# Kernel optimization log

Measured on AMD Instinct MI355X. Metric: run time of the kernel, lower is better.

## Reference

```python
import jax, jax.numpy as jnp
import numpy as np

B, L, H = 2, 1024, 1024   # batch, seq_len, hidden_size
NH, D, K = 16, 64, 4      # num_heads, head_dim, conv kernel
HD = NH * D


def setup_inputs() -> dict:
    key = jax.random.key(0)
    ks = jax.random.split(key, 12)
    s = 0.02  # LeCun-ish init scale as in the torch module
    return {
        "hidden_states": jax.random.normal(ks[0], (B, L, H), jnp.float32),
        "Wq": jax.random.normal(ks[1], (HD, H), jnp.float32) * s,
        "bq": jnp.zeros((HD,), jnp.float32),
        "Wk": jax.random.normal(ks[2], (HD, H), jnp.float32) * s,
        "bk": jnp.zeros((HD,), jnp.float32),
        "Wv": jax.random.normal(ks[3], (HD, H), jnp.float32) * s,
        "bv": jnp.zeros((HD,), jnp.float32),
        "Wa": jax.random.normal(ks[4], (NH, H), jnp.float32) * s,
        "Wb": jax.random.normal(ks[5], (NH, H), jnp.float32) * s,
        "Wconv": jax.random.normal(ks[6], (HD, 1, K), jnp.float32) * s,
        "Wo": jax.random.normal(ks[7], (H, HD), jnp.float32) * s,
        "bo": jnp.zeros((H,), jnp.float32),
    }


def _gated_delta(q, k, v, alpha, beta):
    # q,k,v: [B,L,NH,D]; alpha,beta: [B,L,NH]
    # S_t = S_{t-1} @ (alpha_t * (I - beta_t k_t k_t^T)) + beta_t v_t k_t^T ; o_t = S_t q_t
    eye = jnp.eye(q.shape[-1], dtype=q.dtype)

    def step(S, xs):
        q_t, k_t, v_t, a_t, b_t = xs  # [B,NH,D], [B,NH]
        kk = jnp.einsum('bhd,bhe->bhde', k_t, k_t)
        decay = a_t[..., None, None] * (eye - b_t[..., None, None] * kk)
        S = jnp.einsum('bhde,bhef->bhdf', S, decay) \
            + b_t[..., None, None] * jnp.einsum('bhd,bhe->bhde', v_t, k_t)
        o_t = jnp.einsum('bhde,bhe->bhd', S, q_t)
        return S, o_t

    xs = (jnp.moveaxis(q, 1, 0), jnp.moveaxis(k, 1, 0), jnp.moveaxis(v, 1, 0),
          jnp.moveaxis(alpha, 1, 0), jnp.moveaxis(beta, 1, 0))
    S0 = jnp.zeros((q.shape[0], q.shape[2], q.shape[3], q.shape[3]), q.dtype)
    _, outs = jax.lax.scan(step, S0, xs)  # [L,B,NH,D]
    return jnp.transpose(outs, (1, 2, 0, 3))  # [B,NH,L,D] (matches torch stack+transposes)


def reference(hidden_states, Wq, bq, Wk, bk, Wv, bv, Wa, Wb, Wconv, Wo, bo):
    Bc, Lc, Hc = hidden_states.shape
    q = (hidden_states @ Wq.T + bq).reshape(Bc, Lc, NH, D)
    k = (hidden_states @ Wk.T + bk).reshape(Bc, Lc, NH, D)
    v = (hidden_states @ Wv.T + bv).reshape(Bc, Lc, NH, D)
    alpha = jax.nn.sigmoid(hidden_states @ Wa.T)   # [B,L,NH]
    beta = jax.nn.softplus(hidden_states @ Wb.T)   # [B,L,NH]

    out = _gated_delta(q, k, v, alpha, beta)       # [B,NH,L,D]
    out = out.reshape(Bc, Lc, NH * D)              # replicates torch's reshape of [B,NH,L,D]
    x = jnp.transpose(out, (0, 2, 1))              # [B,HD,L]
    conv = jax.lax.conv_general_dilated(
        x, Wconv, window_strides=(1,), padding=[(K - 1, 0)],
        feature_group_count=NH * D, dimension_numbers=('NCH', 'OIH', 'NCH'))
    x = x + conv                                   # residual depthwise causal conv
    x = jnp.transpose(x, (0, 2, 1))                # [B,L,HD]
    return x @ Wo.T + bo                           # [B,L,H]; dropout is identity at eval
```

## Files before the change

### kernel.cpp

```cpp
#include <hip/hip_runtime.h>
#include <math.h>

#define BB 2
#define LL 1024
#define HH 1024
#define NH 16
#define DD 64
#define HD (NH * DD)
#define MM (BB * LL)
#define RCT 32
#define KEXT 3072
#define NBK 1088

typedef _Float16 f16x8 __attribute__((ext_vector_type(8)));
typedef _Float16 f16x4 __attribute__((ext_vector_type(4)));
typedef float f32x4 __attribute__((ext_vector_type(4)));

__device__ __forceinline__ void load_lds16(const void* g, void* l) {
    __builtin_amdgcn_global_load_lds(
        (const __attribute__((address_space(1))) void*)g,
        (__attribute__((address_space(3))) void*)l, 16, 0, 0);
}

__global__ __launch_bounds__(256) void convert_front(
    const float* __restrict__ hs,
    const float* __restrict__ Wq, const float* __restrict__ Wk,
    const float* __restrict__ Wv, const float* __restrict__ Wa,
    const float* __restrict__ Wb, const float* __restrict__ Wo,
    _Float16* __restrict__ Ae3,
    _Float16* __restrict__ Bk, _Float16* __restrict__ Bqv,
    _Float16* __restrict__ Be2)
{
    const int blk = blockIdx.x;
    const int t = threadIdx.x;

    if (blk < 2048) {
        float4 x = *(const float4*)(hs + (size_t)blk * 1024 + t * 4);
        x.x *= 16.f; x.y *= 16.f; x.z *= 16.f; x.w *= 16.f;
        f16x4 h, l;
        h[0] = (_Float16)x.x; l[0] = (_Float16)(x.x - (float)h[0]);
        h[1] = (_Float16)x.y; l[1] = (_Float16)(x.y - (float)h[1]);
        h[2] = (_Float16)x.z; l[2] = (_Float16)(x.z - (float)h[2]);
        h[3] = (_Float16)x.w; l[3] = (_Float16)(x.w - (float)h[3]);
        _Float16* base = Ae3 + (size_t)blk * KEXT + t * 4;
        *(f16x4*)(base)        = h;
        *(f16x4*)(base + 1024) = l;
        *(f16x4*)(base + 2048) = h;
        return;
    }
    if (blk < 3136) {
        const int n = blk - 2048;
        const float* src = nullptr;
        if (n < 1024)      src = Wk + (size_t)n * 1024;
        else if (n < 1040) src = Wa + (size_t)(n - 1024) * 1024;
        else if (n < 1056) src = Wb + (size_t)(n - 1040) * 1024;
        float4 x = src ? *(const float4*)(src + t * 4)
                       : make_float4(0.f, 0.f, 0.f, 0.f);
        x.x *= 64.f; x.y *= 64.f; x.z *= 64.f; x.w *= 64.f;
        f16x4 h, l;
        h[0] = (_Float16)x.x; l[0] = (_Float16)(x.x - (float)h[0]);
        h[1] = (_Float16)x.y; l[1] = (_Float16)(x.y - (float)h[1]);
        h[2] = (_Float16)x.z; l[2] = (_Float16)(x.z - (float)h[2]);
        h[3] = (_Float16)x.w; l[3] = (_Float16)(x.w - (float)h[3]);
        _Float16* base = Bk + (size_t)n * KEXT + t * 4;
        *(f16x4*)(base)        = h;
        *(f16x4*)(base + 1024) = h;
        *(f16x4*)(base + 2048) = l;
        return;
    }
    if (blk < 5184) {
        const int n = blk - 3136;
        const float* src = (n < 1024) ? Wq + (size_t)n * 1024
                                      : Wv + (size_t)(n - 1024) * 1024;
        float4 x = *(const float4*)(src + t * 4);
        f16x4 h;
        h[0] = (_Float16)(x.x * 64.f);
        h[1] = (_Float16)(x.y * 64.f);
        h[2] = (_Float16)(x.z * 64.f);
        h[3] = (_Float16)(x.w * 64.f);
        *(f16x4*)(Bqv + (size_t)n * 1024 + t * 4) = h;
        return;
    }
    {
        const int n = blk - 5184;
        float4 x = *(const float4*)(Wo + (size_t)n * 1024 + t * 4);
        f16x4 h;
        h[0] = (_Float16)(x.x * 64.f);
        h[1] = (_Float16)(x.y * 64.f);
        h[2] = (_Float16)(x.z * 64.f);
        h[3] = (_Float16)(x.w * 64.f);
        *(f16x4*)(Be2 + (size_t)n * 1024 + t * 4) = h;
    }
}

__global__ __launch_bounds__(256) void mfma_gemm_proj(
    const _Float16* __restrict__ Ae3, const _Float16* __restrict__ Bk,
    const _Float16* __restrict__ Bqv,
    float* __restrict__ qkv, float* __restrict__ ab,
    const float* __restrict__ bq, const float* __restrict__ bk,
    const float* __restrict__ bv)
{
    __shared__ __align__(16) _Float16 As[2][128 * 32];
    __shared__ __align__(16) _Float16 Bs[2][128 * 32];

    const int blk = blockIdx.x;
    const int tid = threadIdx.x;
    const int wave = tid >> 6;
    const int lane = tid & 63;
    const int srow = lane >> 2;
    const int scol = (lane & 3) * 8;
    const int fm = lane & 15;
    const int fq = (lane >> 4) * 8;
    const int rquad = (lane >> 4) * 4;

    if (blk < 272) {
        const int bm = (blk / 17) * 128;
        const int bn = (blk % 17) * 64;
        const int wr = (wave >> 1) * 64;
        const int wc = (wave & 1) * 32;

        const _Float16* gA0 = Ae3 + (size_t)(bm + wave * 32 + srow) * KEXT + scol;
        const _Float16* gA1 = gA0 + (size_t)16 * KEXT;
        const _Float16* gB0 = Bk + (size_t)(bn + wave * 16 + srow) * KEXT + scol;
        _Float16* lA0_0 = &As[0][(wave * 32) * 32];
        _Float16* lA1_0 = &As[0][(wave * 32 + 16) * 32];
        _Float16* lB0_0 = &Bs[0][(wave * 16) * 32];
        _Float16* lA0_1 = &As[1][(wave * 32) * 32];
        _Float16* lA1_1 = &As[1][(wave * 32 + 16) * 32];
        _Float16* lB0_1 = &Bs[1][(wave * 16) * 32];

        f32x4 acc[4][2] = {};

        for (int k0 = 0; k0 < KEXT; k0 += 64) {
            load_lds16(gA0 + k0,      lA0_0);
            load_lds16(gA1 + k0,      lA1_0);
            load_lds16(gB0 + k0,      lB0_0);
            load_lds16(gA0 + k0 + 32, lA0_1);
            load_lds16(gA1 + k0 + 32, lA1_1);
            load_lds16(gB0 + k0 + 32, lB0_1);
            __syncthreads();

            #pragma unroll
            for (int s = 0; s < 2; ++s) {
                f16x8 a[4], b[2];
                #pragma unroll
                for (int mt = 0; mt < 4; ++mt)
                    a[mt] = *(const f16x8*)&As[s][(wr + mt * 16 + fm) * 32 + fq];
                #pragma unroll
                for (int nt = 0; nt < 2; ++nt)
                    b[nt] = *(const f16x8*)&Bs[s][(wc + nt * 16 + fm) * 32 + fq];
                #pragma unroll
                for (int mt = 0; mt < 4; ++mt)
                    #pragma unroll
                    for (int nt = 0; nt < 2; ++nt)
                        acc[mt][nt] = __builtin_amdgcn_mfma_f32_16x16x32_f16(
                            a[mt], b[nt], acc[mt][nt], 0, 0, 0);
            }
            __syncthreads();
        }

        #pragma unroll
        for (int mt = 0; mt < 4; ++mt) {
            #pragma unroll
            for (int nt = 0; nt < 2; ++nt) {
                const int col = bn + wc + nt * 16 + fm;
                #pragma unroll
                for (int i = 0; i < 4; ++i) {
                    const int row = bm + wr + mt * 16 + rquad + i;
                    float val = acc[mt][nt][i] * (1.0f / 1024.0f);
                    if (col < 1024)
                        qkv[(size_t)row * 3072 + 1024 + col] = val + bk[col];
                    else if (col < 1040)
                        ab[(size_t)row * 32 + (col - 1024)] =
                            1.f / (1.f + expf(-val));
                    else if (col < 1056)
                        ab[(size_t)row * 32 + 16 + (col - 1040)] =
                            fmaxf(val, 0.f) + log1pf(expf(-fabsf(val)));
                }
            }
        }
    } else {
        const int n = blk - 272;
        const int bm = (n / 16) * 128;
        const int bn = (n % 16) * 128;
        const int wr = (wave >> 1) * 64;
        const int wc = (wave & 1) * 64;

        const _Float16* gA0 = Ae3 + (size_t)(bm + wave * 32 + srow) * KEXT + scol;
        const _Float16* gA1 = gA0 + (size_t)16 * KEXT;
        const _Float16* gB0 = Bqv + (size_t)(bn + wave * 32 + srow) * 1024 + scol;
        const _Float16* gB1 = gB0 + (size_t)16 * 1024;
        _Float16* lA0_0 = &As[0][(wave * 32) * 32];
        _Float16* lA1_0 = &As[0][(wave * 32 + 16) * 32];
        _Float16* lB0_0 = &Bs[0][(wave * 32) * 32];
        _Float16* lB1_0 = &Bs[0][(wave * 32 + 16) * 32];
        _Float16* lA0_1 = &As[1][(wave * 32) * 32];
        _Float16* lA1_1 = &As[1][(wave * 32 + 16) * 32];
        _Float16* lB0_1 = &Bs[1][(wave * 32) * 32];
        _Float16* lB1_1 = &Bs[1][(wave * 32 + 16) * 32];

        f32x4 acc[4][4] = {};

        for (int k0 = 0; k0 < 1024; k0 += 64) {
            load_lds16(gA0 + k0,      lA0_0);
            load_lds16(gA1 + k0,      lA1_0);
            load_lds16(gB0 + k0,      lB0_0);
            load_lds16(gB1 + k0,      lB1_0);
            load_lds16(gA0 + k0 + 32, lA0_1);
            load_lds16(gA1 + k0 + 32, lA1_1);
            load_lds16(gB0 + k0 + 32, lB0_1);
            load_lds16(gB1 + k0 + 32, lB1_1);
            __syncthreads();

            #pragma unroll
            for (int s = 0; s < 2; ++s) {
                f16x8 a[4], b[4];
                #pragma unroll
                for (int mt = 0; mt < 4; ++mt)
                    a[mt] = *(const f16x8*)&As[s][(wr + mt * 16 + fm) * 32 + fq];
                #pragma unroll
                for (int nt = 0; nt < 4; ++nt)
                    b[nt] = *(const f16x8*)&Bs[s][(wc + nt * 16 + fm) * 32 + fq];
                #pragma unroll
                for (int mt = 0; mt < 4; ++mt)
                    #pragma unroll
                    for (int nt = 0; nt < 4; ++nt)
                        acc[mt][nt] = __builtin_amdgcn_mfma_f32_16x16x32_f16(
                            a[mt], b[nt], acc[mt][nt], 0, 0, 0);
            }
            __syncthreads();
        }

        #pragma unroll
        for (int mt = 0; mt < 4; ++mt) {
            #pragma unroll
            for (int nt = 0; nt < 4; ++nt) {
                const int col = bn + wc + nt * 16 + fm;
                #pragma unroll
                for (int i = 0; i < 4; ++i) {
                    const int row = bm + wr + mt * 16 + rquad + i;
                    float val = acc[mt][nt][i] * (1.0f / 1024.0f);
                    if (col < 1024)
                        qkv[(size_t)row * 3072 + col] = val + bq[col];
                    else
                        qkv[(size_t)row * 3072 + 1024 + col] = val + bv[col - 1024];
                }
            }
        }
    }
}

__global__ __launch_bounds__(256) void mfma_gemm_out(
    const _Float16* __restrict__ Ae2, const _Float16* __restrict__ Be2,
    float* __restrict__ outp, const float* __restrict__ bo)
{
    __shared__ __align__(16) _Float16 As[2][128 * 32];
    __shared__ __align__(16) _Float16 Bs[2][64 * 32];

    const int tid = threadIdx.x;
    const int wave = tid >> 6;
    const int lane = tid & 63;
    const int bm = blockIdx.y * 128;
    const int bn = blockIdx.x * 64;
    const int wr = (wave >> 1) * 64;
    const int wc = (wave & 1) * 32;

    const int srow = lane >> 2;
    const int scol = (lane & 3) * 8;
    const _Float16* gA0 = Ae2 + (size_t)(bm + wave * 32 + srow) * 1024 + scol;
    const _Float16* gA1 = gA0 + (size_t)16 * 1024;
    const _Float16* gB0 = Be2 + (size_t)(bn + wave * 16 + srow) * 1024 + scol;
    _Float16* lA0_0 = &As[0][(wave * 32) * 32];
    _Float16* lA1_0 = &As[0][(wave * 32 + 16) * 32];
    _Float16* lB0_0 = &Bs[0][(wave * 16) * 32];
    _Float16* lA0_1 = &As[1][(wave * 32) * 32];
    _Float16* lA1_1 = &As[1][(wave * 32 + 16) * 32];
    _Float16* lB0_1 = &Bs[1][(wave * 16) * 32];

    const int fm = lane & 15;
    const int fq = (lane >> 4) * 8;

    f32x4 acc[4][2] = {};

    for (int k0 = 0; k0 < 1024; k0 += 64) {
        load_lds16(gA0 + k0,      lA0_0);
        load_lds16(gA1 + k0,      lA1_0);
        load_lds16(gB0 + k0,      lB0_0);
        load_lds16(gA0 + k0 + 32, lA0_1);
        load_lds16(gA1 + k0 + 32, lA1_1);
        load_lds16(gB0 + k0 + 32, lB0_1);
        __syncthreads();

        #pragma unroll
        for (int s = 0; s < 2; ++s) {
            f16x8 a[4], b[2];
            #pragma unroll
            for (int mt = 0; mt < 4; ++mt)
                a[mt] = *(const f16x8*)&As[s][(wr + mt * 16 + fm) * 32 + fq];
            #pragma unroll
            for (int nt = 0; nt < 2; ++nt)
                b[nt] = *(const f16x8*)&Bs[s][(wc + nt * 16 + fm) * 32 + fq];
            #pragma unroll
            for (int mt = 0; mt < 4; ++mt)
                #pragma unroll
                for (int nt = 0; nt < 2; ++nt)
                    acc[mt][nt] = __builtin_amdgcn_mfma_f32_16x16x32_f16(
                        a[mt], b[nt], acc[mt][nt], 0, 0, 0);
        }
        __syncthreads();
    }

    const int rquad = (lane >> 4) * 4;
    #pragma unroll
    for (int mt = 0; mt < 4; ++mt) {
        #pragma unroll
        for (int nt = 0; nt < 2; ++nt) {
            const int col = bn + wc + nt * 16 + fm;
            #pragma unroll
            for (int i = 0; i < 4; ++i) {
                const int row = bm + wr + mt * 16 + rquad + i;
                outp[(size_t)row * 1024 + col] = acc[mt][nt][i] * 64.f + bo[col];
            }
        }
    }
}

template <int CTRL>
__device__ __forceinline__ float dpp_addf(float x) {
    int y = __builtin_amdgcn_update_dpp(0, __builtin_bit_cast(int, x),
                                        CTRL, 0xF, 0xF, true);
    return x + __builtin_bit_cast(float, y);
}
__device__ __forceinline__ float red16(float x) {
    x = dpp_addf<0xB1>(x);
    x = dpp_addf<0x4E>(x);
    x = dpp_addf<0x124>(x);
    x = dpp_addf<0x128>(x);
    return x;
}

__global__ __launch_bounds__(64) void gdn_recurrence(
    const float* __restrict__ qkv, const float* __restrict__ ab,
    float* __restrict__ att)
{
    __shared__ __align__(16) float ks[2][RCT][64];
    __shared__ __align__(16) float qs[2][RCT][64];
    __shared__ __align__(16) float vs_[2][RCT][4];
    __shared__ __align__(16) float gab[2][RCT][2];

    const int blk = blockIdx.x;
    const int bh = blk & 31;
    const int s  = blk >> 5;
    const int b  = bh >> 4;
    const int h  = bh & 15;
    const int lane = threadIdx.x;
    const int rl = lane >> 4;
    const int el = lane & 15;
    const int e0 = el * 4;
    const int r0 = s * 4;

    const float* qb  = qkv + (size_t)b * LL * 3072 + h * 64;
    const float* kb  = qb + 1024;
    const float* vb  = qb + 2048 + r0;
    const float* abp = ab + (size_t)b * LL * 32 + h;
    float* op = att + ((size_t)(b * NH + h) * DD + r0 + rl) * LL;

    const int st = lane >> 4;
    const int sd = (lane & 15) * 4;

    float S0 = 0.f, S1 = 0.f, S2 = 0.f, S3 = 0.f;

    {
        const size_t ro = (size_t)st * 3072 + sd;
        #pragma unroll
        for (int m = 0; m < 8; ++m) {
            load_lds16(kb + ro + (size_t)m * 4 * 3072, &ks[0][m * 4][0]);
            load_lds16(qb + ro + (size_t)m * 4 * 3072, &qs[0][m * 4][0]);
        }
        float4 pv = make_float4(0.f,0.f,0.f,0.f);
        if (lane < RCT) pv = *(const float4*)(vb + (size_t)lane * 3072);
        float pab = (lane < 32) ? abp[(size_t)lane * 32]
                                : abp[(size_t)(lane - 32) * 32 + 16];
        if (lane < RCT) *(float4*)&vs_[0][lane][0] = pv;
        if (lane < 32) gab[0][lane][0] = pab;
        else           gab[0][lane - 32][1] = pab;
    }
    __syncthreads();

    const int NCHUNK = LL / RCT;
    for (int c = 0; c < NCHUNK; ++c) {
        const int cur = c & 1, nxt = cur ^ 1;
        const bool more = (c + 1 < NCHUNK);

        float4 pv = make_float4(0.f,0.f,0.f,0.f);
        float pab = 0.f;
        if (more) {
            const size_t t0 = (size_t)(c + 1) * RCT;
            const size_t ro = (t0 + st) * 3072 + sd;
            #pragma unroll
            for (int m = 0; m < 8; ++m) {
                load_lds16(kb + ro + (size_t)m * 4 * 3072, &ks[nxt][m * 4][0]);
                load_lds16(qb + ro + (size_t)m * 4 * 3072, &qs[nxt][m * 4][0]);
            }
            if (lane < RCT) pv = *(const float4*)(vb + (t0 + lane) * 3072);
            pab = (lane < 32) ? abp[(t0 + lane) * 32]
                              : abp[(t0 + lane - 32) * 32 + 16];
        }

        float4 kr[4], qr[4];
        float vr[4];
        float2 abr[4];
        #pragma unroll
        for (int i = 0; i < 2; ++i) {
            kr[i] = *(const float4*)&ks[cur][i][e0];
            qr[i] = *(const float4*)&qs[cur][i][e0];
            vr[i] = vs_[cur][i][rl];
            abr[i] = *(const float2*)&gab[cur][i][0];
        }

        float o0 = 0.f, o1 = 0.f, o2 = 0.f;
        #pragma unroll 4
        for (int t = 0; t < RCT; ++t) {
            const int tf = (t + 2 < RCT) ? t + 2 : RCT - 1;
            kr[(t + 2) & 3] = *(const float4*)&ks[cur][tf][e0];
            qr[(t + 2) & 3] = *(const float4*)&qs[cur][tf][e0];
            vr[(t + 2) & 3] = vs_[cur][tf][rl];
            abr[(t + 2) & 3] = *(const float2*)&gab[cur][tf][0];

            const float4 kc = kr[t & 3];
            const float4 qc = qr[t & 3];
            const float vc = vr[t & 3];
            const float ac = abr[t & 3].x;
            const float bc = abr[t & 3].y;

            float p0 = fmaf(S1, kc.y, S0 * kc.x);
            float p1 = fmaf(S3, kc.w, S2 * kc.z);
            float sk = red16(p0 + p1);

            const float cf = bc * fmaf(-ac, sk, vc);

            S0 = fmaf(ac, S0, cf * kc.x);
            S1 = fmaf(ac, S1, cf * kc.y);
            S2 = fmaf(ac, S2, cf * kc.z);
            S3 = fmaf(ac, S3, cf * kc.w);

            float q0 = fmaf(S1, qc.y, S0 * qc.x);
            float q1 = fmaf(S3, qc.w, S2 * qc.z);
            float o = red16(q0 + q1);

            const int ph = t & 3;
            if (ph == 0) o0 = o;
            else if (ph == 1) o1 = o;
            else if (ph == 2) o2 = o;
            else if (el == 0)
                *(float4*)(op + c * RCT + t - 3) = make_float4(o0, o1, o2, o);
        }

        if (more) {
            if (lane < RCT) *(float4*)&vs_[nxt][lane][0] = pv;
            if (lane < 32) gab[nxt][lane][0] = pab;
            else           gab[nxt][lane - 32][1] = pab;
        }
        __syncthreads();
    }
}

__global__ __launch_bounds__(256) void conv_convert(
    const float* __restrict__ att, const float* __restrict__ Wconv,
    _Float16* __restrict__ Ae2)
{
    __shared__ float yt[112][68];
    const int lb = blockIdx.x;
    const int h  = blockIdx.y;
    const int b  = blockIdx.z;
    const int tid = threadIdx.x;

    {
        const int d = tid >> 2;
        const int part = tid & 3;
        const float* src  = att + ((size_t)(b * NH + h) * DD + d) * LL;
        const float* srcm = src - (size_t)DD * LL;
        #pragma unroll
        for (int m = 0; m < 7; ++m) {
            const int off = (part * 7 + m) * 4;
            const int lg = lb * 64 - 48 + off;
            float4 v;
            if (lg >= 0)      v = *(const float4*)(src + lg);
            else if (h > 0)   v = *(const float4*)(srcm + lg + 1024);
            else              v = make_float4(0.f, 0.f, 0.f, 0.f);
            yt[off + 0][d] = v.x; yt[off + 1][d] = v.y;
            yt[off + 2][d] = v.z; yt[off + 3][d] = v.w;
        }
    }
    __syncthreads();

    float4 w[4];
    #pragma unroll
    for (int k = 0; k < 4; ++k)
        w[k] = ((const float4*)Wconv)[tid * 4 + k];

    const int d0 = (tid & 15) * 4;
    const int lq = tid >> 4;
    const float sc = 1.f / 4096.f;

    #pragma unroll
    for (int rr = 0; rr < 4; ++rr) {
        const int ll = rr * 16 + lq;
        float y0[4], y1[4], y2[4], y3[4];
        *(float4*)y0 = *(const float4*)&yt[ll +  0][d0];
        *(float4*)y1 = *(const float4*)&yt[ll + 16][d0];
        *(float4*)y2 = *(const float4*)&yt[ll + 32][d0];
        *(float4*)y3 = *(const float4*)&yt[ll + 48][d0];
        f16x4 hi;
        #pragma unroll
        for (int k = 0; k < 4; ++k) {
            float acc = y3[k];
            acc = fmaf(w[k].x, y0[k], acc);
            acc = fmaf(w[k].y, y1[k], acc);
            acc = fmaf(w[k].z, y2[k], acc);
            acc = fmaf(w[k].w, y3[k], acc);
            hi[k] = (_Float16)(acc * sc);
        }
        const size_t row = (size_t)b * 1024 + h * 64 + lb * 4 + rr;
        *(f16x4*)(Ae2 + row * 1024 + tid * 4) = hi;
    }
}

extern "C" void kernel_launch(void* const* d_in, const int* in_sizes, int n_in,
                              void* d_out, int out_size, void* d_ws, size_t ws_size,
                              hipStream_t stream)
{
    const float* hs    = (const float*)d_in[0];
    const float* Wq    = (const float*)d_in[1];
    const float* bq    = (const float*)d_in[2];
    const float* Wk    = (const float*)d_in[3];
    const float* bk    = (const float*)d_in[4];
    const float* Wv    = (const float*)d_in[5];
    const float* bv    = (const float*)d_in[6];
    const float* Wa    = (const float*)d_in[7];
    const float* Wb    = (const float*)d_in[8];
    const float* Wconv = (const float*)d_in[9];
    const float* Wo    = (const float*)d_in[10];
    const float* bo    = (const float*)d_in[11];
    float* out = (float*)d_out;

    char* w = (char*)d_ws;
    float* qkv = (float*)w;        w += (size_t)MM * 3072 * 4;
    float* att = (float*)w;        w += (size_t)MM * 1024 * 4;
    float* ab  = (float*)w;        w += (size_t)MM * 32 * 4;
    _Float16* Ae3 = (_Float16*)w;  w += (size_t)MM * KEXT * 2;
    _Float16* Bk  = (_Float16*)w;  w += (size_t)NBK * KEXT * 2;
    _Float16* Bqv = (_Float16*)w;  w += (size_t)2048 * 1024 * 2;
    _Float16* Ae2 = (_Float16*)w;  w += (size_t)MM * 1024 * 2;
    _Float16* Be2 = (_Float16*)w;  w += (size_t)1024 * 1024 * 2;

    hipLaunchKernelGGL(convert_front, dim3(6208), dim3(256), 0, stream,
                       hs, Wq, Wk, Wv, Wa, Wb, Wo, Ae3, Bk, Bqv, Be2);

    hipLaunchKernelGGL(mfma_gemm_proj, dim3(528), dim3(256), 0, stream,
                       Ae3, Bk, Bqv, qkv, ab, bq, bk, bv);

    hipLaunchKernelGGL(gdn_recurrence, dim3(512), dim3(64), 0, stream, qkv, ab, att);

    hipLaunchKernelGGL(conv_convert, dim3(16, 16, BB), dim3(256), 0, stream,
                       att, Wconv, Ae2);

    hipLaunchKernelGGL(mfma_gemm_out, dim3(1024 / 64, MM / 128), dim3(256), 0, stream,
                       Ae2, Be2, out, bo);
}
```

Before: 292.8 us.

## Double-buffer LDS tiles to prefetch next K-step during MFMA compute

In the projection and output GEMM kernels, the LDS tiles become two ping-pong sets. The loads for the next 64-wide K step are issued before the MFMA work on the current step, so global-to-LDS traffic overlaps with compute instead of stalling at a barrier every iteration. The cost is twice the LDS per block (64 KB in the projection kernel), which may lower occupancy. The end-of-iteration barrier now also waits on the prefetch.

Measured after the change: 297.9 us. No clear change (+1.7%).

```diff
diff --git a/kernel.cpp b/kernel.cpp
--- a/kernel.cpp
+++ b/kernel.cpp
@@ -100,8 +100,8 @@
     const float* __restrict__ bq, const float* __restrict__ bk,
     const float* __restrict__ bv)
 {
-    __shared__ __align__(16) _Float16 As[2][128 * 32];
-    __shared__ __align__(16) _Float16 Bs[2][128 * 32];
+    __shared__ __align__(16) _Float16 As[2][2][128 * 32];
+    __shared__ __align__(16) _Float16 Bs[2][2][128 * 32];
 
     const int blk = blockIdx.x;
     const int tid = threadIdx.x;
@@ -122,33 +122,45 @@
         const _Float16* gA0 = Ae3 + (size_t)(bm + wave * 32 + srow) * KEXT + scol;
         const _Float16* gA1 = gA0 + (size_t)16 * KEXT;
         const _Float16* gB0 = Bk + (size_t)(bn + wave * 16 + srow) * KEXT + scol;
-        _Float16* lA0_0 = &As[0][(wave * 32) * 32];
-        _Float16* lA1_0 = &As[0][(wave * 32 + 16) * 32];
-        _Float16* lB0_0 = &Bs[0][(wave * 16) * 32];
-        _Float16* lA0_1 = &As[1][(wave * 32) * 32];
-        _Float16* lA1_1 = &As[1][(wave * 32 + 16) * 32];
-        _Float16* lB0_1 = &Bs[1][(wave * 16) * 32];
+
+        _Float16* lA0 = &As[0][0][(wave * 32) * 32];
+        _Float16* lA1 = &As[0][0][(wave * 32 + 16) * 32];
+        _Float16* lB0 = &Bs[0][0][(wave * 16) * 32];
+        const size_t setStride = (size_t)2 * 128 * 32;
+        const size_t slcStride = (size_t)128 * 32;
 
         f32x4 acc[4][2] = {};
 
-        for (int k0 = 0; k0 < KEXT; k0 += 64) {
-            load_lds16(gA0 + k0,      lA0_0);
-            load_lds16(gA1 + k0,      lA1_0);
-            load_lds16(gB0 + k0,      lB0_0);
-            load_lds16(gA0 + k0 + 32, lA0_1);
-            load_lds16(gA1 + k0 + 32, lA1_1);
-            load_lds16(gB0 + k0 + 32, lB0_1);
-            __syncthreads();
-
+        #pragma unroll
+        for (int s = 0; s < 2; ++s) {
+            load_lds16(gA0 + s * 32, lA0 + s * slcStride);
+            load_lds16(gA1 + s * 32, lA1 + s * slcStride);
+            load_lds16(gB0 + s * 32, lB0 + s * slcStride);
+        }
+        __syncthreads();
+
+        const int NI = KEXT / 64;
+        for (int i = 0; i < NI; ++i) {
+            const int cur = i & 1;
+            if (i + 1 < NI) {
+                const int k1 = (i + 1) * 64;
+                const size_t off = (size_t)(cur ^ 1) * setStride;
+                #pragma unroll
+                for (int s = 0; s < 2; ++s) {
+                    load_lds16(gA0 + k1 + s * 32, lA0 + off + s * slcStride);
+                    load_lds16(gA1 + k1 + s * 32, lA1 + off + s * slcStride);
+                    load_lds16(gB0 + k1 + s * 32, lB0 + off + s * slcStride);
+                }
+            }
             #pragma unroll
             for (int s = 0; s < 2; ++s) {
                 f16x8 a[4], b[2];
                 #pragma unroll
                 for (int mt = 0; mt < 4; ++mt)
-                    a[mt] = *(const f16x8*)&As[s][(wr + mt * 16 + fm) * 32 + fq];
+                    a[mt] = *(const f16x8*)&As[cur][s][(wr + mt * 16 + fm) * 32 + fq];
                 #pragma unroll
                 for (int nt = 0; nt < 2; ++nt)
-                    b[nt] = *(const f16x8*)&Bs[s][(wc + nt * 16 + fm) * 32 + fq];
+                    b[nt] = *(const f16x8*)&Bs[cur][s][(wc + nt * 16 + fm) * 32 + fq];
                 #pragma unroll
                 for (int mt = 0; mt < 4; ++mt)
                     #pragma unroll
@@ -190,37 +202,48 @@
         const _Float16* gA1 = gA0 + (size_t)16 * KEXT;
         const _Float16* gB0 = Bqv + (size_t)(bn + wave * 32 + srow) * 1024 + scol;
         const _Float16* gB1 = gB0 + (size_t)16 * 1024;
-        _Float16* lA0_0 = &As[0][(wave * 32) * 32];
-        _Float16* lA1_0 = &As[0][(wave * 32 + 16) * 32];
-        _Float16* lB0_0 = &Bs[0][(wave * 32) * 32];
-        _Float16* lB1_0 = &Bs[0][(wave * 32 + 16) * 32];
-        _Float16* lA0_1 = &As[1][(wave * 32) * 32];
-        _Float16* lA1_1 = &As[1][(wave * 32 + 16) * 32];
-        _Float16* lB0_1 = &Bs[1][(wave * 32) * 32];
-        _Float16* lB1_1 = &Bs[1][(wave * 32 + 16) * 32];
+
+        _Float16* lA0 = &As[0][0][(wave * 32) * 32];
+        _Float16* lA1 = &As[0][0][(wave * 32 + 16) * 32];
+        _Float16* lB0 = &Bs[0][0][(wave * 32) * 32];
+        _Float16* lB1 = &Bs[0][0][(wave * 32 + 16) * 32];
+        const size_t setStride = (size_t)2 * 128 * 32;
+        const size_t slcStride = (size_t)128 * 32;
 
         f32x4 acc[4][4] = {};
 
-        for (int k0 = 0; k0 < 1024; k0 += 64) {
-            load_lds16(gA0 + k0,      lA0_0);
-            load_lds16(gA1 + k0,      lA1_0);
-            load_lds16(gB0 + k0,      lB0_0);
-            load_lds16(gB1 + k0,      lB1_0);
-            load_lds16(gA0 + k0 + 32, lA0_1);
-            load_lds16(gA1 + k0 + 32, lA1_1);
-            load_lds16(gB0 + k0 + 32, lB0_1);
-            load_lds16(gB1 + k0 + 32, lB1_1);
-            __syncthreads();
-
+        #pragma unroll
+        for (int s = 0; s < 2; ++s) {
+            load_lds16(gA0 + s * 32, lA0 + s * slcStride);
+            load_lds16(gA1 + s * 32, lA1 + s * slcStride);
+            load_lds16(gB0 + s * 32, lB0 + s * slcStride);
+            load_lds16(gB1 + s * 32, lB1 + s * slcStride);
+        }
+        __syncthreads();
+
+        const int NI = 1024 / 64;
+        for (int i = 0; i < NI; ++i) {
+            const int cur = i & 1;
+            if (i + 1 < NI) {
+                const int k1 = (i + 1) * 64;
+                const size_t off = (size_t)(cur ^ 1) * setStride;
+                #pragma unroll
+                for (int s = 0; s < 2; ++s) {
+                    load_lds16(gA0 + k1 + s * 32, lA0 + off + s * slcStride);
+                    load_lds16(gA1 + k1 + s * 32, lA1 + off + s * slcStride);
+                    load_lds16(gB0 + k1 + s * 32, lB0 + off + s * slcStride);
+                    load_lds16(gB1 + k1 + s * 32, lB1 + off + s * slcStride);
+                }
+            }
             #pragma unroll
             for (int s = 0; s < 2; ++s) {
                 f16x8 a[4], b[4];
                 #pragma unroll
                 for (int mt = 0; mt < 4; ++mt)
-                    a[mt] = *(const f16x8*)&As[s][(wr + mt * 16 + fm) * 32 + fq];
+                    a[mt] = *(const f16x8*)&As[cur][s][(wr + mt * 16 + fm) * 32 + fq];
                 #pragma unroll
                 for (int nt = 0; nt < 4; ++nt)
-                    b[nt] = *(const f16x8*)&Bs[s][(wc + nt * 16 + fm) * 32 + fq];
+                    b[nt] = *(const f16x8*)&Bs[cur][s][(wc + nt * 16 + fm) * 32 + fq];
                 #pragma unroll
                 for (int mt = 0; mt < 4; ++mt)
                     #pragma unroll
@@ -254,8 +277,8 @@
     const _Float16* __restrict__ Ae2, const _Float16* __restrict__ Be2,
     float* __restrict__ outp, const float* __restrict__ bo)
 {
-    __shared__ __align__(16) _Float16 As[2][128 * 32];
-    __shared__ __align__(16) _Float16 Bs[2][64 * 32];
+    __shared__ __align__(16) _Float16 As[2][2][128 * 32];
+    __shared__ __align__(16) _Float16 Bs[2][2][64 * 32];
 
     const int tid = threadIdx.x;
     const int wave = tid >> 6;
@@ -270,36 +293,52 @@
     const _Float16* gA0 = Ae2 + (size_t)(bm + wave * 32 + srow) * 1024 + scol;
     const _Float16* gA1 = gA0 + (size_t)16 * 1024;
     const _Float16* gB0 = Be2 + (size_t)(bn + wave * 16 + srow) * 1024 + scol;
-    _Float16* lA0_0 = &As[0][(wave * 32) * 32];
-    _Float16* lA1_0 = &As[0][(wave * 32 + 16) * 32];
-    _Float16* lB0_0 = &Bs[0][(wave * 16) * 32];
-    _Float16* lA0_1 = &As[1][(wave * 32) * 32];
-    _Float16* lA1_1 = &As[1][(wave * 32 + 16) * 32];
-    _Float16* lB0_1 = &Bs[1][(wave * 16) * 32];
+
+    _Float16* lA0 = &As[0][0][(wave * 32) * 32];
+    _Float16* lA1 = &As[0][0][(wave * 32 + 16) * 32];
+    _Float16* lB0 = &Bs[0][0][(wave * 16) * 32];
+    const size_t setStrideA = (size_t)2 * 128 * 32;
+    const size_t slcStrideA = (size_t)128 * 32;
+    const size_t setStrideB = (size_t)2 * 64 * 32;
+    const size_t slcStrideB = (size_t)64 * 32;
 
     const int fm = lane & 15;
     const int fq = (lane >> 4) * 8;
 
     f32x4 acc[4][2] = {};
 
-    for (int k0 = 0; k0 < 1024; k0 += 64) {
-        load_lds16(gA0 + k0,      lA0_0);
-        load_lds16(gA1 + k0,      lA1_0);
-        load_lds16(gB0 + k0,      lB0_0);
-        load_lds16(gA0 + k0 + 32, lA0_1);
-        load_lds16(gA1 + k0 + 32, lA1_1);
-        load_lds16(gB0 + k0 + 32, lB0_1);
-        __syncthreads();
-
+    #pragma unroll
+    for (int s = 0; s < 2; ++s) {
+        load_lds16(gA0 + s * 32, lA0 + s * slcStrideA);
+        load_lds16(gA1 + s * 32, lA1 + s * slcStrideA);
+        load_lds16(gB0 + s * 32, lB0 + s * slcStrideB);
+    }
+    __syncthreads();
+
+    const int NI = 1024 / 64;
+    for (int i = 0; i < NI; ++i) {
+        const int cur = i & 1;
+        if (i + 1 < NI) {
+            const int k1 = (i + 1) * 64;
+            #pragma unroll
+            for (int s = 0; s < 2; ++s) {
+                load_lds16(gA0 + k1 + s * 32,
+                           lA0 + (size_t)(cur ^ 1) * setStrideA + s * slcStrideA);
+                load_lds16(gA1 + k1 + s * 32,
+                           lA1 + (size_t)(cur ^ 1) * setStrideA + s * slcStrideA);
+                load_lds16(gB0 + k1 + s * 32,
+                           lB0 + (size_t)(cur ^ 1) * setStrideB + s * slcStrideB);
+            }
+        }
         #pragma unroll
         for (int s = 0; s < 2; ++s) {
             f16x8 a[4], b[2];
             #pragma unroll
             for (int mt = 0; mt < 4; ++mt)
-                a[mt] = *(const f16x8*)&As[s][(wr + mt * 16 + fm) * 32 + fq];
+                a[mt] = *(const f16x8*)&As[cur][s][(wr + mt * 16 + fm) * 32 + fq];
             #pragma unroll
             for (int nt = 0; nt < 2; ++nt)
-                b[nt] = *(const f16x8*)&Bs[s][(wc + nt * 16 + fm) * 32 + fq];
+                b[nt] = *(const f16x8*)&Bs[cur][s][(wc + nt * 16 + fm) * 32 + fq];
             #pragma unroll
             for (int mt = 0; mt < 4; ++mt)
                 #pragma unroll
```
